# Performance work log

Measured on AMD Instinct MI355X. Metric: run time of the kernel, lower is better.

The kernel has to match this reference:

```python
import jax, jax.numpy as jnp
import numpy as np

N_X_AXIS = 128
N_Y_AXIS = 128
X_RANGE = (-2.0, 2.0)
Y_RANGE = (-2.0, 2.0)
BATCH = 4
N_CTX = 1024


def make_grid():
    # Give_2d_Grid: flattened (n_x*n_y, 2) grid, x-major (consistent with
    # the view(batch, n_x_axis, n_y_axis, 3) reshape in forward).
    gx = jnp.linspace(X_RANGE[0], X_RANGE[1], N_X_AXIS, dtype=jnp.float32)
    gy = jnp.linspace(Y_RANGE[0], Y_RANGE[1], N_Y_AXIS, dtype=jnp.float32)
    xx, yy = jnp.meshgrid(gx, gy, indexing='ij')  # (n_x, n_y)
    return jnp.stack([xx.ravel(), yy.ravel()], axis=-1)  # (n_x*n_y, 2)


def setup_inputs() -> dict:
    key = jax.random.key(0)
    k1, k2 = jax.random.split(key)
    X = jax.random.normal(k1, (BATCH, N_CTX, 2), dtype=jnp.float32)
    Y = jax.random.normal(k2, (BATCH, N_CTX, 2), dtype=jnp.float32)
    grid = make_grid()
    return {"X": X, "Y": Y, "grid": grid}


def reference(X, Y, grid):
    # RBF Gram matrix between grid points and context points X.
    # k(a,b) = exp(-||a-b||^2 / (2 l^2)), l = 1 (default length scale).
    # d2: (B, G, n)
    d2 = jnp.sum((grid[None, :, None, :] - X[:, None, :, :]) ** 2, axis=-1)
    Gram = jnp.exp(-0.5 * d2)  # (B, G, n)

    # Psi: prepend a column of ones -> (B, n, 3)
    ones = jnp.ones(Y.shape[:2] + (1,), dtype=Y.dtype)
    Expand_Y = jnp.concatenate([ones, Y], axis=-1)

    # Feature map: (B, G, 3)
    FM = jnp.einsum('bgn,bnc->bgc', Gram, Expand_Y)

    # Density-normalize the value channels by the density channel.
    density = FM[..., 0:1]
    FM = jnp.concatenate([density, FM[..., 1:] / density], axis=-1)

    # (B, G, 3) -> (B, n_x, n_y, 3) -> (B, 3, n_y, n_x)
    out = FM.reshape(X.shape[0], N_X_AXIS, N_Y_AXIS, 3)
    return out.transpose(0, 3, 2, 1)
```

## Files before the change

kernel.cpp:

```cpp
#include <hip/hip_runtime.h>


#define NCTX 1024

typedef float    f32x4 __attribute__((ext_vector_type(4)));
typedef _Float16 f16x8 __attribute__((ext_vector_type(8)));

__device__ __forceinline__ float fast_exp2(float x) {
#if __has_builtin(__builtin_amdgcn_exp2f)
  return __builtin_amdgcn_exp2f(x);
#else
  return exp2f(x);
#endif
}

__global__ __launch_bounds__(512) void convcnp_fused_kernel(
    const float* __restrict__ X,
    const float* __restrict__ Y,
    const float* __restrict__ grid,
    float* __restrict__ out)
{
  __shared__ float4 xy[NCTX];
  __shared__ unsigned char panel[4 * 8192];
  __shared__ f32x4 den[4][64];

  const int t = threadIdx.x;
  const int w = t >> 6, l = t & 63;
  const int bid = blockIdx.x;
  const int b = bid >> 4, jyt = (bid >> 2) & 3, ixt = bid & 3;

  const float SC = 0.84932180028801907f;

  const float2* Xb = (const float2*)X + b * NCTX;
  const float2* Yb = (const float2*)Y + b * NCTX;
#pragma unroll
  for (int k = 0; k < 2; ++k) {
    int n = t + 512 * k;
    float2 x = Xb[n];
    float2 y = Yb[n];
    xy[n] = make_float4(x.x * SC, x.y * SC, y.x, y.y);
  }

  const int r  = t & 31;
  const int g8 = t >> 5;
  const float gxs = grid[(ixt * 32 + r) * 256] * SC;
  const float gys = grid[2 * (jyt * 32 + r) + 1] * SC;
  const int wbase = ((r * 256 + g8 * 16) ^ ((r & 15) << 4));

  const int trc = w & 3, tr = trc >> 1, tc = trc & 1;
  const int cA = (w < 4) ? 0 : 1;
  const int row16 = l & 15, kg = l >> 4;
  const int arow = tr * 16 + row16, brow = tc * 16 + row16;
  const int aswz = (arow & 15) << 4, bswz = (brow & 15) << 4;

  f32x4 accA = {0.f, 0.f, 0.f, 0.f};
  f32x4 accB = {0.f, 0.f, 0.f, 0.f};

  __syncthreads();

  for (int q = 0; q < 8; ++q) {
    const int n0 = q * 128 + g8 * 8;
    f16x8 ve, v0, v1, vx;
#pragma unroll
    for (int j = 0; j < 8; ++j) {
      float4 v = xy[n0 + j];
      float dx = gxs - v.x;
      float ex = fast_exp2(-(dx * dx));
      float dy = gys - v.y;
      float ey = fast_exp2(-(dy * dy));
      ve[j] = (_Float16)ey;
      v0[j] = (_Float16)(ey * v.z);
      v1[j] = (_Float16)(ey * v.w);
      vx[j] = (_Float16)ex;
    }
    *(f16x8*)(panel + 0 * 8192 + wbase) = ve;
    *(f16x8*)(panel + 1 * 8192 + wbase) = v0;
    *(f16x8*)(panel + 2 * 8192 + wbase) = v1;
    *(f16x8*)(panel + 3 * 8192 + wbase) = vx;
    __syncthreads();

    const unsigned char* Ap = panel + cA * 8192;
    const unsigned char* A2 = panel + 2 * 8192;
    const unsigned char* Bp = panel + 3 * 8192;
#pragma unroll
    for (int kk = 0; kk < 4; ++kk) {
      const int kb = kk * 64 + kg * 16;
      f16x8 af = *(const f16x8*)(Ap + ((arow * 256 + kb) ^ aswz));
      f16x8 bf = *(const f16x8*)(Bp + ((brow * 256 + kb) ^ bswz));
      accA = __builtin_amdgcn_mfma_f32_16x16x32_f16(af, bf, accA, 0, 0, 0);
      if (w < 4) {
        f16x8 a2 = *(const f16x8*)(A2 + ((arow * 256 + kb) ^ aswz));
        accB = __builtin_amdgcn_mfma_f32_16x16x32_f16(a2, bf, accB, 0, 0, 0);
      }
    }
    __syncthreads();
  }

  const int jy0 = jyt * 32 + tr * 16 + kg * 4;
  const int ix  = ixt * 32 + tc * 16 + row16;
  float* ob = out + b * 3 * 16384;
  if (w < 4) {
    den[w][l] = accA;
#pragma unroll
    for (int g = 0; g < 4; ++g) {
      const int o = (jy0 + g) * 128 + ix;
      ob[o]             = accA[g];
      ob[2 * 16384 + o] = accB[g] / accA[g];
    }
  }
  __syncthreads();
  if (w >= 4) {
    f32x4 d = den[w - 4][l];
#pragma unroll
    for (int g = 0; g < 4; ++g) {
      const int o = (jy0 + g) * 128 + ix;
      ob[1 * 16384 + o] = accA[g] / d[g];
    }
  }
}

extern "C" void kernel_launch(void* const* d_in, const int* in_sizes, int n_in,
                              void* d_out, int out_size, void* d_ws, size_t ws_size,
                              hipStream_t stream) {
  const float* X    = (const float*)d_in[0];
  const float* Y    = (const float*)d_in[1];
  const float* grid = (const float*)d_in[2];
  float* out        = (float*)d_out;

  convcnp_fused_kernel<<<dim3(64), dim3(512), 0, stream>>>(X, Y, grid, out);
}
```

Before: 65.25 us.

## Shrink output tiles to 16x16 and split K across waves with reduction

The kernel now uses 256 blocks of 256 threads, each computing a 16x16 output tile instead of 32x32, so four times as many blocks occupy the GPU's compute units. Each wave handles a different K-slice of the context panel and runs three MFMAs per step; results are summed through shared memory at the end. The context array in shared memory is padded to avoid bank conflicts. In exchange, the exp work per output rises because each block recomputes the separable exponentials for smaller tiles, and a final cross-wave reduction is added.

```diff
diff --git a/kernel.cpp b/kernel.cpp
--- a/kernel.cpp
+++ b/kernel.cpp
@@ -14,47 +14,48 @@
 #endif
 }
 
-__global__ __launch_bounds__(512) void convcnp_fused_kernel(
+__device__ __forceinline__ int xyi(int n) { return n + (n >> 3); }
+
+__global__ __launch_bounds__(256) void convcnp_fused256(
     const float* __restrict__ X,
     const float* __restrict__ Y,
     const float* __restrict__ grid,
     float* __restrict__ out)
 {
-  __shared__ float4 xy[NCTX];
-  __shared__ unsigned char panel[4 * 8192];
-  __shared__ f32x4 den[4][64];
+  __shared__ float4 xy[NCTX + NCTX / 8];
+  __shared__ unsigned char panel[4 * 4096];
+  __shared__ f32x4 red[4][3][64];
 
   const int t = threadIdx.x;
   const int w = t >> 6, l = t & 63;
   const int bid = blockIdx.x;
-  const int b = bid >> 4, jyt = (bid >> 2) & 3, ixt = bid & 3;
+  const int b = bid >> 6, jyt = (bid >> 3) & 7, ixt = bid & 7;
 
   const float SC = 0.84932180028801907f;
 
   const float2* Xb = (const float2*)X + b * NCTX;
   const float2* Yb = (const float2*)Y + b * NCTX;
 #pragma unroll
-  for (int k = 0; k < 2; ++k) {
-    int n = t + 512 * k;
+  for (int k = 0; k < 4; ++k) {
+    int n = t + 256 * k;
     float2 x = Xb[n];
     float2 y = Yb[n];
-    xy[n] = make_float4(x.x * SC, x.y * SC, y.x, y.y);
+    xy[xyi(n)] = make_float4(x.x * SC, x.y * SC, y.x, y.y);
   }
 
-  const int r  = t & 31;
-  const int g8 = t >> 5;
-  const float gxs = grid[(ixt * 32 + r) * 256] * SC;
-  const float gys = grid[2 * (jyt * 32 + r) + 1] * SC;
-  const int wbase = ((r * 256 + g8 * 16) ^ ((r & 15) << 4));
+  const int r  = t & 15;
+  const int g8 = t >> 4;
+  const float gxs = grid[(ixt * 16 + r) * 256] * SC;
+  const float gys = grid[2 * (jyt * 16 + r) + 1] * SC;
+  const int wbase = (r * 256 + g8 * 16) ^ (r << 4);
 
-  const int trc = w & 3, tr = trc >> 1, tc = trc & 1;
-  const int cA = (w < 4) ? 0 : 1;
   const int row16 = l & 15, kg = l >> 4;
-  const int arow = tr * 16 + row16, brow = tc * 16 + row16;
-  const int aswz = (arow & 15) << 4, bswz = (brow & 15) << 4;
+  const int kb   = w * 64 + kg * 16;
+  const int aoff = (row16 * 256 + kb) ^ (row16 << 4);
 
-  f32x4 accA = {0.f, 0.f, 0.f, 0.f};
-  f32x4 accB = {0.f, 0.f, 0.f, 0.f};
+  f32x4 acc0 = {0.f, 0.f, 0.f, 0.f};
+  f32x4 acc1 = {0.f, 0.f, 0.f, 0.f};
+  f32x4 acc2 = {0.f, 0.f, 0.f, 0.f};
 
   __syncthreads();
 
@@ -63,58 +64,52 @@
     f16x8 ve, v0, v1, vx;
 #pragma unroll
     for (int j = 0; j < 8; ++j) {
-      float4 v = xy[n0 + j];
+      float4 v = xy[xyi(n0 + j)];
       float dx = gxs - v.x;
+      float dy = gys - v.y;
       float ex = fast_exp2(-(dx * dx));
-      float dy = gys - v.y;
       float ey = fast_exp2(-(dy * dy));
       ve[j] = (_Float16)ey;
       v0[j] = (_Float16)(ey * v.z);
       v1[j] = (_Float16)(ey * v.w);
       vx[j] = (_Float16)ex;
     }
-    *(f16x8*)(panel + 0 * 8192 + wbase) = ve;
-    *(f16x8*)(panel + 1 * 8192 + wbase) = v0;
-    *(f16x8*)(panel + 2 * 8192 + wbase) = v1;
-    *(f16x8*)(panel + 3 * 8192 + wbase) = vx;
+    *(f16x8*)(panel + 0 * 4096 + wbase) = ve;
+    *(f16x8*)(panel + 1 * 4096 + wbase) = v0;
+    *(f16x8*)(panel + 2 * 4096 + wbase) = v1;
+    *(f16x8*)(panel + 3 * 4096 + wbase) = vx;
     __syncthreads();
 
-    const unsigned char* Ap = panel + cA * 8192;
-    const unsigned char* A2 = panel + 2 * 8192;
-    const unsigned char* Bp = panel + 3 * 8192;
-#pragma unroll
-    for (int kk = 0; kk < 4; ++kk) {
-      const int kb = kk * 64 + kg * 16;
-      f16x8 af = *(const f16x8*)(Ap + ((arow * 256 + kb) ^ aswz));
-      f16x8 bf = *(const f16x8*)(Bp + ((brow * 256 + kb) ^ bswz));
-      accA = __builtin_amdgcn_mfma_f32_16x16x32_f16(af, bf, accA, 0, 0, 0);
-      if (w < 4) {
-        f16x8 a2 = *(const f16x8*)(A2 + ((arow * 256 + kb) ^ aswz));
-        accB = __builtin_amdgcn_mfma_f32_16x16x32_f16(a2, bf, accB, 0, 0, 0);
-      }
-    }
+    f16x8 ae = *(const f16x8*)(panel + 0 * 4096 + aoff);
+    f16x8 a0 = *(const f16x8*)(panel + 1 * 4096 + aoff);
+    f16x8 a1 = *(const f16x8*)(panel + 2 * 4096 + aoff);
+    f16x8 bx = *(const f16x8*)(panel + 3 * 4096 + aoff);
+    acc0 = __builtin_amdgcn_mfma_f32_16x16x32_f16(ae, bx, acc0, 0, 0, 0);
+    acc1 = __builtin_amdgcn_mfma_f32_16x16x32_f16(a0, bx, acc1, 0, 0, 0);
+    acc2 = __builtin_amdgcn_mfma_f32_16x16x32_f16(a1, bx, acc2, 0, 0, 0);
     __syncthreads();
   }
 
-  const int jy0 = jyt * 32 + tr * 16 + kg * 4;
-  const int ix  = ixt * 32 + tc * 16 + row16;
-  float* ob = out + b * 3 * 16384;
-  if (w < 4) {
-    den[w][l] = accA;
+  red[w][0][l] = acc0;
+  red[w][1][l] = acc1;
+  red[w][2][l] = acc2;
+  __syncthreads();
+
+  if (w == 0) {
+    f32x4 s0 = red[0][0][l] + red[1][0][l] + red[2][0][l] + red[3][0][l];
+    f32x4 s1 = red[0][1][l] + red[1][1][l] + red[2][1][l] + red[3][1][l];
+    f32x4 s2 = red[0][2][l] + red[1][2][l] + red[2][2][l] + red[3][2][l];
+    f32x4 o1 = s1 / s0;
+    f32x4 o2 = s2 / s0;
+    const int ix  = ixt * 16 + row16;
+    const int jy0 = jyt * 16 + kg * 4;
+    float* ob = out + b * 3 * 16384;
 #pragma unroll
     for (int g = 0; g < 4; ++g) {
       const int o = (jy0 + g) * 128 + ix;
-      ob[o]             = accA[g];
-      ob[2 * 16384 + o] = accB[g] / accA[g];
-    }
-  }
-  __syncthreads();
-  if (w >= 4) {
-    f32x4 d = den[w - 4][l];
-#pragma unroll
-    for (int g = 0; g < 4; ++g) {
-      const int o = (jy0 + g) * 128 + ix;
-      ob[1 * 16384 + o] = accA[g] / d[g];
+      ob[o]             = s0[g];
+      ob[1 * 16384 + o] = o1[g];
+      ob[2 * 16384 + o] = o2[g];
     }
   }
 }
@@ -127,5 +122,5 @@
   const float* grid = (const float*)d_in[2];
   float* out        = (float*)d_out;
 
-  convcnp_fused_kernel<<<dim3(64), dim3(512), 0, stream>>>(X, Y, grid, out);
+  convcnp_fused256<<<dim3(256), dim3(256), 0, stream>>>(X, Y, grid, out);
 }
```

Result: faster. 61.47 us (-5.8%).
